# Kernel tuning notes

Measured on AMD Instinct MI355X. Metric: run time of the kernel, lower is better.

Reference implementation:

```python
import jax, jax.numpy as jnp
import numpy as np

NUM_GROUPS = 32
EPS = 1e-5


def group_norm(x, gamma, beta):
    # x: (b, c, h, w)
    b, c, h, w = x.shape
    xg = x.reshape(b, NUM_GROUPS, c // NUM_GROUPS, h, w)
    mean = xg.mean(axis=(2, 3, 4), keepdims=True)
    var = xg.var(axis=(2, 3, 4), keepdims=True)
    xn = ((xg - mean) * jax.lax.rsqrt(var + EPS)).reshape(b, c, h, w)
    return xn * gamma[None, :, None, None] + beta[None, :, None, None]


def conv1x1(x, w, b):
    # 1x1 conv == channel matmul: x (b,c,h,w), w (out,in), b (out,)
    return jnp.einsum('bchw,oc->bohw', x, w) + b[None, :, None, None]


def setup_inputs() -> dict:
    key = jax.random.key(0)
    ks = jax.random.split(key, 10)
    C = 512
    x = jax.random.normal(ks[0], (16, C, 32, 32), dtype=jnp.float32)
    s = 1.0 / np.sqrt(C)
    return {
        'x': x,
        'norm_w': jnp.ones((C,), jnp.float32),
        'norm_b': jnp.zeros((C,), jnp.float32),
        'q_w': jax.random.normal(ks[1], (C, C), jnp.float32) * s,
        'q_b': jax.random.normal(ks[2], (C,), jnp.float32) * 0.01,
        'k_w': jax.random.normal(ks[3], (C, C), jnp.float32) * s,
        'k_b': jax.random.normal(ks[4], (C,), jnp.float32) * 0.01,
        'v_w': jax.random.normal(ks[5], (C, C), jnp.float32) * s,
        'v_b': jax.random.normal(ks[6], (C,), jnp.float32) * 0.01,
        'proj_w': jax.random.normal(ks[7], (C, C), jnp.float32) * s,
        'proj_b': jax.random.normal(ks[8], (C,), jnp.float32) * 0.01,
    }


def reference(x, norm_w, norm_b, q_w, q_b, k_w, k_b, v_w, v_b, proj_w, proj_b):
    b, c, h, w = x.shape
    hn = group_norm(x, norm_w, norm_b)
    q = conv1x1(hn, q_w, q_b).reshape(b, c, h * w)  # (b, c, n)
    k = conv1x1(hn, k_w, k_b).reshape(b, c, h * w)
    v = conv1x1(hn, v_w, v_b).reshape(b, c, h * w)
    scale = jnp.float32(c) ** -0.5
    # scores[b, i, j] = sum_c q[b,c,i] * k[b,c,j]
    scores = jnp.einsum('bci,bcj->bij', q, k) * scale  # (b, n, n)
    attn = jax.nn.softmax(scores, axis=-1)
    # h_[b, c, i] = sum_j v[b,c,j] * attn[b,i,j]
    out = jnp.einsum('bcj,bij->bci', v, attn).reshape(b, c, h, w)
    return x + conv1x1(out, proj_w, proj_b)
```

## Files before the change

kernel.cpp:

```cpp
#include <hip/hip_runtime.h>

#define B_ 16
#define C_ 512
#define N_ 1024

typedef __attribute__((ext_vector_type(8))) short bf16x8_t;
typedef __attribute__((ext_vector_type(4))) float f32x4_t;

__device__ __forceinline__ unsigned short f2bf(float f) {
  unsigned int u = __float_as_uint(f);
  u += 0x7fffu + ((u >> 16) & 1u);
  return (unsigned short)(u >> 16);
}

__device__ __forceinline__ f32x4_t mfma16(bf16x8_t a, bf16x8_t b, f32x4_t c) {
  return __builtin_amdgcn_mfma_f32_16x16x32_bf16(a, b, c, 0, 0, 0);
}

__device__ __forceinline__ void gload_lds16(const void* g, void* l) {
  __builtin_amdgcn_global_load_lds(
      (const __attribute__((address_space(1))) unsigned int*)g,
      (__attribute__((address_space(3))) unsigned int*)l, 16, 0, 0);
}

__global__ __launch_bounds__(256) void castw_k(
    const float* __restrict__ qw, const float* __restrict__ kw,
    const float* __restrict__ vw, const float* __restrict__ pw,
    unsigned short* __restrict__ Wqkv, unsigned short* __restrict__ Wp) {
  int i = blockIdx.x * 256 + threadIdx.x;
  Wqkv[i] = f2bf(qw[i]);
  Wqkv[262144 + i] = f2bf(kw[i]);
  Wqkv[524288 + i] = f2bf(vw[i]);
  Wp[i] = f2bf(pw[i]);
}

__global__ __launch_bounds__(512, 1) void gn_fused_k(
    const float* __restrict__ x, const float* __restrict__ gw,
    const float* __restrict__ gb, unsigned short* __restrict__ hn) {
  int blk = blockIdx.x;
  int b = blk >> 4, gp = blk & 15;
  int t = threadIdx.x, lane = t & 63, wave = t >> 6;
  __shared__ float xs[32768];
  __shared__ float red[2][2][8];
  const float* xg = x + ((long)b * C_ + gp * 32) * N_;
  float s0 = 0.f, s20 = 0.f, s1 = 0.f, s21 = 0.f;
#pragma unroll
  for (int i = 0; i < 16; ++i) {
    int f4 = t + 512 * i;
    float4 v = ((const float4*)xg)[f4];
    float sum = v.x + v.y + v.z + v.w;
    float sq = v.x * v.x + v.y * v.y + v.z * v.z + v.w * v.w;
    if (i < 8) { s0 += sum; s20 += sq; } else { s1 += sum; s21 += sq; }
    int fi = f4 << 2;
    int c = fi >> 10, n = fi & 1023;
    int nx = n ^ (((c >> 3) & 3) << 4);
    *(float4*)&xs[(c << 10) + nx] = v;
  }
#pragma unroll
  for (int m = 1; m < 64; m <<= 1) {
    s0 += __shfl_xor(s0, m); s20 += __shfl_xor(s20, m);
    s1 += __shfl_xor(s1, m); s21 += __shfl_xor(s21, m);
  }
  if (lane == 0) {
    red[0][0][wave] = s0; red[1][0][wave] = s20;
    red[0][1][wave] = s1; red[1][1][wave] = s21;
  }
  __syncthreads();
  float m0 = 0.f, v0 = 0.f, m1 = 0.f, v1 = 0.f;
#pragma unroll
  for (int w = 0; w < 8; ++w) {
    m0 += red[0][0][w]; v0 += red[1][0][w];
    m1 += red[0][1][w]; v1 += red[1][1][w];
  }
  m0 *= (1.f / 16384.f); m1 *= (1.f / 16384.f);
  float rv0 = rsqrtf(v0 * (1.f / 16384.f) - m0 * m0 + 1e-5f);
  float rv1 = rsqrtf(v1 * (1.f / 16384.f) - m1 * m1 + 1e-5f);
  int q = t & 3;
  float mean = (q >> 1) ? m1 : m0, rv = (q >> 1) ? rv1 : rv0;
  float ga[8], be[8];
#pragma unroll
  for (int jj = 0; jj < 8; ++jj) {
    int gc = gp * 32 + q * 8 + jj;
    ga[jj] = gw[gc] * rv;
    be[jj] = gb[gc] - mean * ga[jj];
  }
  unsigned short* ob = hn + (long)b * N_ * C_ + gp * 32 + q * 8;
  int n0 = t >> 2;
  for (int it = 0; it < 8; ++it) {
    int n = n0 + (it << 7);
    int nsw = n ^ (q << 4);
    unsigned short us[8];
#pragma unroll
    for (int jj = 0; jj < 8; ++jj) {
      int c = q * 8 + jj;
      us[jj] = f2bf(xs[(c << 10) + nsw] * ga[jj] + be[jj]);
    }
    *(uint4*)(ob + (long)n * C_) = *(uint4*)us;
  }
}

__global__ __launch_bounds__(256) void gemm_qkv(
    const unsigned short* __restrict__ W, const unsigned short* __restrict__ HN,
    const float* __restrict__ qb, const float* __restrict__ kb,
    const float* __restrict__ vb, unsigned short* __restrict__ Q2,
    unsigned short* __restrict__ K2, unsigned short* __restrict__ V2,
    float scale) {
  int flat = blockIdx.x + 12 * (blockIdx.y + 8 * blockIdx.z);
  int nf = (flat & 7) * 192 + (flat >> 3);
  int bxi = nf % 12, rem = nf / 12;
  int byi = rem & 7, bz = rem >> 3;
  const unsigned short* Ab = W + (long)bxi * 128 * 512;
  const unsigned short* Bb = HN + (long)bz * N_ * C_ + (long)byi * 128 * 512;
  __shared__ char lds[32768];
  char* As = lds;
  char* Bs = lds + 16384;
  int tid = threadIdx.x;
  int lane = tid & 63, wave = tid >> 6;
  int wr = wave >> 1, wc = wave & 1;
  int lrow = lane & 15, kgrp = lane >> 4;
  f32x4_t acc[4][4];
#pragma unroll
  for (int i = 0; i < 4; ++i)
#pragma unroll
    for (int j = 0; j < 4; ++j) acc[i][j] = (f32x4_t){0.f, 0.f, 0.f, 0.f};

  int perm = (((lane & 7) ^ (lane >> 3)) << 3);
  const unsigned short* Asrc = Ab + (long)(wave * 32 + (lane >> 3)) * 512 + perm;
  const unsigned short* Bsrc = Bb + (long)(wave * 32 + (lane >> 3)) * 512 + perm;
  char* Adst = As + wave * 32 * 128;
  char* Bdst = Bs + wave * 32 * 128;

  for (int kt = 0; kt < 8; ++kt) {
    __syncthreads();
#pragma unroll
    for (int i = 0; i < 4; ++i) {
      gload_lds16(Asrc + (long)i * 8 * 512 + kt * 64, Adst + i * 1024);
      gload_lds16(Bsrc + (long)i * 8 * 512 + kt * 64, Bdst + i * 1024);
    }
    __syncthreads();
#pragma unroll
    for (int ks = 0; ks < 2; ++ks) {
      bf16x8_t af[4], bfv[4];
#pragma unroll
      for (int mi = 0; mi < 4; ++mi) {
        int r = wr * 64 + mi * 16 + lrow;
        int o = r * 128 + ks * 64 + kgrp * 16;
        o ^= (r & 7) << 4;
        af[mi] = *(bf16x8_t*)(As + o);
      }
#pragma unroll
      for (int ni = 0; ni < 4; ++ni) {
        int r = wc * 64 + ni * 16 + lrow;
        int o = r * 128 + ks * 64 + kgrp * 16;
        o ^= (r & 7) << 4;
        bfv[ni] = *(bf16x8_t*)(Bs + o);
      }
#pragma unroll
      for (int mi = 0; mi < 4; ++mi)
#pragma unroll
        for (int ni = 0; ni < 4; ++ni)
          acc[mi][ni] = mfma16(af[mi], bfv[ni], acc[mi][ni]);
    }
  }

  int slab = bxi >> 2;
  const float* bias = slab == 0 ? qb : (slab == 1 ? kb : vb);
  float scl = slab == 0 ? scale : 1.f;
  int rowloc = (bxi & 3) * 128 + wr * 64;
  int colbase = byi * 128 + wc * 64;
  unsigned short* ob =
      (slab == 0 ? Q2 : (slab == 1 ? K2 : V2)) + ((long)bz << 19);
#pragma unroll
  for (int mi = 0; mi < 4; ++mi) {
#pragma unroll
    for (int ni = 0; ni < 4; ++ni) {
      int row0 = rowloc + mi * 16 + kgrp * 4;
      int col = colbase + ni * 16 + lrow;
      unsigned short us[4];
#pragma unroll
      for (int rg = 0; rg < 4; ++rg)
        us[rg] = f2bf((acc[mi][ni][rg] + bias[row0 + rg]) * scl);
      if (slab < 2) {
        long off = ((long)(col >> 4) << 13) + ((long)(row0 >> 3) << 7) +
                   ((col & 15) << 3) + (row0 & 7);
        *(ushort4*)(ob + off) = make_ushort4(us[0], us[1], us[2], us[3]);
      } else {
        long base16 = ((long)(row0 >> 4) << 14) + ((long)(col >> 3) << 7) +
                      (col & 7) + (row0 & 15) * 8;
#pragma unroll
        for (int rg = 0; rg < 4; ++rg) ob[base16 + rg * 8] = us[rg];
      }
    }
  }
}

__global__ __launch_bounds__(512, 1) void attn_pv_k(
    const unsigned short* __restrict__ q2, const unsigned short* __restrict__ k2,
    const unsigned short* __restrict__ v2, unsigned short* __restrict__ ao) {
  int f = blockIdx.x;
  int b = f & 15, ib = f >> 4;
  int tid = threadIdx.x, lane = tid & 63, wave = tid >> 6;
  int lrow = lane & 15, kgrp = lane >> 4;
  __shared__ unsigned short P2[65536];
  __shared__ float red[2][8][64];
  {
    const unsigned short* qsrc =
        q2 + ((long)b << 19) + ((long)(ib * 4) << 13) + wave * 4096 + lane * 8;
    char* qdst = (char*)P2 + wave * 8192;
#pragma unroll
    for (int i = 0; i < 8; ++i) gload_lds16(qsrc + i * 512, qdst + i * 1024);
  }
  asm volatile("s_waitcnt vmcnt(0)" ::: "memory");
  __syncthreads();
  f32x4_t acc[4][8];
#pragma unroll
  for (int h = 0; h < 4; ++h)
#pragma unroll
    for (int t = 0; t < 8; ++t) acc[h][t] = (f32x4_t){0.f, 0.f, 0.f, 0.f};
  const unsigned short* kb =
      k2 + ((long)b << 19) + ((long)(wave * 8) << 13) + lane * 8;
  for (int ks = 0; ks < 16; ++ks) {
    bf16x8_t kf[8];
#pragma unroll
    for (int t = 0; t < 8; ++t)
      kf[t] = *(const bf16x8_t*)(kb + t * 8192 + ks * 512);
    bf16x8_t qa[4];
#pragma unroll
    for (int h = 0; h < 4; ++h)
      qa[h] = *(const bf16x8_t*)&P2[h * 8192 + ks * 512 + lane * 8];
    __builtin_amdgcn_s_setprio(1);
#pragma unroll
    for (int h = 0; h < 4; ++h)
#pragma unroll
      for (int t = 0; t < 8; ++t) acc[h][t] = mfma16(qa[h], kf[t], acc[h][t]);
    __builtin_amdgcn_s_setprio(0);
  }
  float mx[4][4];
#pragma unroll
  for (int h = 0; h < 4; ++h)
#pragma unroll
    for (int rg = 0; rg < 4; ++rg) mx[h][rg] = -1e30f;
#pragma unroll
  for (int h = 0; h < 4; ++h)
#pragma unroll
    for (int t = 0; t < 8; ++t)
#pragma unroll
      for (int rg = 0; rg < 4; ++rg) mx[h][rg] = fmaxf(mx[h][rg], acc[h][t][rg]);
#pragma unroll
  for (int m = 1; m < 16; m <<= 1)
#pragma unroll
    for (int h = 0; h < 4; ++h)
#pragma unroll
      for (int rg = 0; rg < 4; ++rg)
        mx[h][rg] = fmaxf(mx[h][rg], __shfl_xor(mx[h][rg], m));
  if (lrow == 0) {
#pragma unroll
    for (int h = 0; h < 4; ++h)
#pragma unroll
      for (int rg = 0; rg < 4; ++rg)
        red[0][wave][h * 16 + kgrp * 4 + rg] = mx[h][rg];
  }
  __syncthreads();
  float gm[4][4], sm[4][4];
#pragma unroll
  for (int h = 0; h < 4; ++h)
#pragma unroll
    for (int rg = 0; rg < 4; ++rg) {
      int r = h * 16 + kgrp * 4 + rg;
      float g0 = fmaxf(fmaxf(red[0][0][r], red[0][1][r]),
                       fmaxf(red[0][2][r], red[0][3][r]));
      float g1 = fmaxf(fmaxf(red[0][4][r], red[0][5][r]),
                       fmaxf(red[0][6][r], red[0][7][r]));
      gm[h][rg] = fmaxf(g0, g1);
      sm[h][rg] = 0.f;
    }
#pragma unroll
  for (int h = 0; h < 4; ++h)
#pragma unroll
    for (int t = 0; t < 8; ++t) {
      int j = wave * 128 + t * 16 + lrow;
      int jb = j >> 3;
      int ob = h * 16384 + jb * 128 + (j & 7);
      int cx = (jb & 7) << 3;
#pragma unroll
      for (int rg = 0; rg < 4; ++rg) {
        float p = __expf(acc[h][t][rg] - gm[h][rg]);
        sm[h][rg] += p;
        P2[ob + (((kgrp * 4 + rg) << 3) ^ cx)] = f2bf(p);
      }
    }
#pragma unroll
  for (int m = 1; m < 16; m <<= 1)
#pragma unroll
    for (int h = 0; h < 4; ++h)
#pragma unroll
      for (int rg = 0; rg < 4; ++rg) sm[h][rg] += __shfl_xor(sm[h][rg], m);
  if (lrow == 0) {
#pragma unroll
    for (int h = 0; h < 4; ++h)
#pragma unroll
      for (int rg = 0; rg < 4; ++rg)
        red[1][wave][h * 16 + kgrp * 4 + rg] = sm[h][rg];
  }
  __syncthreads();
  float inv[4][4];
#pragma unroll
  for (int h = 0; h < 4; ++h)
#pragma unroll
    for (int rg = 0; rg < 4; ++rg) {
      int r = h * 16 + kgrp * 4 + rg;
      float s0 = red[1][0][r] + red[1][1][r] + red[1][2][r] + red[1][3][r];
      float s1 = red[1][4][r] + red[1][5][r] + red[1][6][r] + red[1][7][r];
      inv[h][rg] = 1.f / (s0 + s1);
    }
  f32x4_t o[4][4];
#pragma unroll
  for (int h = 0; h < 4; ++h)
#pragma unroll
    for (int cf = 0; cf < 4; ++cf) o[h][cf] = (f32x4_t){0.f, 0.f, 0.f, 0.f};
  const unsigned short* vbp =
      v2 + ((long)b << 19) + ((long)(wave * 4) << 14) + lane * 8;
  for (int js = 0; js < 32; ++js) {
    bf16x8_t vf[4];
#pragma unroll
    for (int cf = 0; cf < 4; ++cf)
      vf[cf] = *(const bf16x8_t*)(vbp + cf * 16384 + js * 512);
    int jb = js * 4 + kgrp;
    int pox = ((lrow ^ (jb & 7)) << 3) + jb * 128;
    bf16x8_t pa[4];
#pragma unroll
    for (int h = 0; h < 4; ++h)
      pa[h] = *(const bf16x8_t*)&P2[h * 16384 + pox];
    __builtin_amdgcn_s_setprio(1);
#pragma unroll
    for (int h = 0; h < 4; ++h)
#pragma unroll
      for (int cf = 0; cf < 4; ++cf)
        o[h][cf] = mfma16(pa[h], vf[cf], o[h][cf]);
    __builtin_amdgcn_s_setprio(0);
  }
  unsigned short* aob = ao + ((long)(b * N_ + ib * 64)) * C_;
#pragma unroll
  for (int h = 0; h < 4; ++h)
#pragma unroll
    for (int cf = 0; cf < 4; ++cf) {
      int c = wave * 64 + cf * 16 + lrow;
#pragma unroll
      for (int rg = 0; rg < 4; ++rg) {
        int i = h * 16 + kgrp * 4 + rg;
        aob[(long)i * C_ + c] = f2bf(o[h][cf][rg] * inv[h][rg]);
      }
    }
}

__global__ __launch_bounds__(256) void gemm_proj(
    const unsigned short* __restrict__ A, const unsigned short* __restrict__ Bm,
    const float* __restrict__ bias, const float* __restrict__ resid,
    float* __restrict__ outp) {
  int flat = blockIdx.x + 4 * (blockIdx.y + 8 * blockIdx.z);
  int nf = (flat & 7) * 64 + (flat >> 3);
  int bxi = nf & 3, byi = (nf >> 2) & 7, bz = nf >> 5;
  const unsigned short* Ab = A + (long)bxi * 128 * 512;
  const unsigned short* Bb = Bm + (long)bz * N_ * C_ + (long)byi * 128 * 512;
  __shared__ char lds[32768];
  char* As = lds;
  char* Bs = lds + 16384;
  int tid = threadIdx.x;
  int lane = tid & 63, wave = tid >> 6;
  int wr = wave >> 1, wc = wave & 1;
  int lrow = lane & 15, kgrp = lane >> 4;
  f32x4_t acc[4][4];
#pragma unroll
  for (int i = 0; i < 4; ++i)
#pragma unroll
    for (int j = 0; j < 4; ++j) acc[i][j] = (f32x4_t){0.f, 0.f, 0.f, 0.f};

  int perm = (((lane & 7) ^ (lane >> 3)) << 3);
  const unsigned short* Asrc = Ab + (long)(wave * 32 + (lane >> 3)) * 512 + perm;
  const unsigned short* Bsrc = Bb + (long)(wave * 32 + (lane >> 3)) * 512 + perm;
  char* Adst = As + wave * 32 * 128;
  char* Bdst = Bs + wave * 32 * 128;

  for (int kt = 0; kt < 8; ++kt) {
    __syncthreads();
#pragma unroll
    for (int i = 0; i < 4; ++i) {
      gload_lds16(Asrc + (long)i * 8 * 512 + kt * 64, Adst + i * 1024);
      gload_lds16(Bsrc + (long)i * 8 * 512 + kt * 64, Bdst + i * 1024);
    }
    __syncthreads();
#pragma unroll
    for (int ks = 0; ks < 2; ++ks) {
      bf16x8_t af[4], bfv[4];
#pragma unroll
      for (int mi = 0; mi < 4; ++mi) {
        int r = wr * 64 + mi * 16 + lrow;
        int o = r * 128 + ks * 64 + kgrp * 16;
        o ^= (r & 7) << 4;
        af[mi] = *(bf16x8_t*)(As + o);
      }
#pragma unroll
      for (int ni = 0; ni < 4; ++ni) {
        int r = wc * 64 + ni * 16 + lrow;
        int o = r * 128 + ks * 64 + kgrp * 16;
        o ^= (r & 7) << 4;
        bfv[ni] = *(bf16x8_t*)(Bs + o);
      }
#pragma unroll
      for (int mi = 0; mi < 4; ++mi)
#pragma unroll
        for (int ni = 0; ni < 4; ++ni)
          acc[mi][ni] = mfma16(af[mi], bfv[ni], acc[mi][ni]);
    }
  }

  int rowbase = bxi * 128 + wr * 64;
  int colbase = byi * 128 + wc * 64;
  float* ob = outp + (long)bz * C_ * N_;
  const float* rb = resid + (long)bz * C_ * N_;
#pragma unroll
  for (int mi = 0; mi < 4; ++mi) {
#pragma unroll
    for (int ni = 0; ni < 4; ++ni) {
      int row0 = rowbase + mi * 16 + kgrp * 4;
      int col = colbase + ni * 16 + lrow;
#pragma unroll
      for (int rg = 0; rg < 4; ++rg) {
        int r = row0 + rg;
        ob[(long)r * N_ + col] =
            acc[mi][ni][rg] + bias[r] + rb[(long)r * N_ + col];
      }
    }
  }
}

extern "C" void kernel_launch(void* const* d_in, const int* in_sizes, int n_in,
                              void* d_out, int out_size, void* d_ws,
                              size_t ws_size, hipStream_t stream) {
  (void)in_sizes; (void)n_in; (void)out_size; (void)ws_size;
  const float* x = (const float*)d_in[0];
  const float* nw = (const float*)d_in[1];
  const float* nb = (const float*)d_in[2];
  const float* qw = (const float*)d_in[3];
  const float* qbias = (const float*)d_in[4];
  const float* kw = (const float*)d_in[5];
  const float* kbias = (const float*)d_in[6];
  const float* vw = (const float*)d_in[7];
  const float* vbias = (const float*)d_in[8];
  const float* pw = (const float*)d_in[9];
  const float* pbias = (const float*)d_in[10];
  float* out = (float*)d_out;

  char* ws = (char*)d_ws;
  unsigned short* WQKV = (unsigned short*)(ws + 0);
  unsigned short* Wp = (unsigned short*)(ws + 1572864);
  unsigned short* HN = (unsigned short*)(ws + 2097152);
  unsigned short* Q2 = (unsigned short*)(ws + 18874368);
  unsigned short* K2 = (unsigned short*)(ws + 35651584);
  unsigned short* V2 = (unsigned short*)(ws + 52428800);
  unsigned short* AO = (unsigned short*)(ws + 69206016);

  castw_k<<<1024, 256, 0, stream>>>(qw, kw, vw, pw, WQKV, Wp);
  gn_fused_k<<<256, 512, 0, stream>>>(x, nw, nb, HN);

  const float scale = 0.04419417382415922f;
  gemm_qkv<<<dim3(12, 8, B_), 256, 0, stream>>>(WQKV, HN, qbias, kbias, vbias,
                                                Q2, K2, V2, scale);
  attn_pv_k<<<256, 512, 0, stream>>>(Q2, K2, V2, AO);
  gemm_proj<<<dim3(4, 8, B_), 256, 0, stream>>>(Wp, AO, pbias, x, out);
}
```

Baseline: 112.9 us.

## Prefetch V fragments, use exp2 with log2e-folded scale, centralize softmax reductions

The PV loop now double-buffers V fragments in registers, loading the next step's data while the current MFMAs run, and is fully unrolled to hide global load latency. The softmax switches from __expf to exp2f, with log2(e) folded into the Q scale constant. The cross-wave max and sum reductions are done once by 64 threads into shared memory instead of redundantly by every thread, which costs two extra barriers. Register pressure rises from the prefetch buffers and the full unroll.

```diff
diff --git a/kernel.cpp b/kernel.cpp
--- a/kernel.cpp
+++ b/kernel.cpp
@@ -203,6 +203,7 @@
   int lrow = lane & 15, kgrp = lane >> 4;
   __shared__ unsigned short P2[65536];
   __shared__ float red[2][8][64];
+  __shared__ float gmr[64], invr[64];
   {
     const unsigned short* qsrc =
         q2 + ((long)b << 19) + ((long)(ib * 4) << 13) + wave * 4096 + lane * 8;
@@ -261,17 +262,19 @@
         red[0][wave][h * 16 + kgrp * 4 + rg] = mx[h][rg];
   }
   __syncthreads();
+  if (tid < 64) {
+    float g = red[0][0][tid];
+#pragma unroll
+    for (int w = 1; w < 8; ++w) g = fmaxf(g, red[0][w][tid]);
+    gmr[tid] = g;
+  }
+  __syncthreads();
   float gm[4][4], sm[4][4];
 #pragma unroll
   for (int h = 0; h < 4; ++h)
 #pragma unroll
     for (int rg = 0; rg < 4; ++rg) {
-      int r = h * 16 + kgrp * 4 + rg;
-      float g0 = fmaxf(fmaxf(red[0][0][r], red[0][1][r]),
-                       fmaxf(red[0][2][r], red[0][3][r]));
-      float g1 = fmaxf(fmaxf(red[0][4][r], red[0][5][r]),
-                       fmaxf(red[0][6][r], red[0][7][r]));
-      gm[h][rg] = fmaxf(g0, g1);
+      gm[h][rg] = gmr[h * 16 + kgrp * 4 + rg];
       sm[h][rg] = 0.f;
     }
 #pragma unroll
@@ -284,7 +287,7 @@
       int cx = (jb & 7) << 3;
 #pragma unroll
       for (int rg = 0; rg < 4; ++rg) {
-        float p = __expf(acc[h][t][rg] - gm[h][rg]);
+        float p = exp2f(acc[h][t][rg] - gm[h][rg]);
         sm[h][rg] += p;
         P2[ob + (((kgrp * 4 + rg) << 3) ^ cx)] = f2bf(p);
       }
@@ -303,28 +306,37 @@
         red[1][wave][h * 16 + kgrp * 4 + rg] = sm[h][rg];
   }
   __syncthreads();
+  if (tid < 64) {
+    float s = red[1][0][tid];
+#pragma unroll
+    for (int w = 1; w < 8; ++w) s += red[1][w][tid];
+    invr[tid] = 1.f / s;
+  }
+  __syncthreads();
   float inv[4][4];
 #pragma unroll
   for (int h = 0; h < 4; ++h)
 #pragma unroll
-    for (int rg = 0; rg < 4; ++rg) {
-      int r = h * 16 + kgrp * 4 + rg;
-      float s0 = red[1][0][r] + red[1][1][r] + red[1][2][r] + red[1][3][r];
-      float s1 = red[1][4][r] + red[1][5][r] + red[1][6][r] + red[1][7][r];
-      inv[h][rg] = 1.f / (s0 + s1);
-    }
+    for (int rg = 0; rg < 4; ++rg)
+      inv[h][rg] = invr[h * 16 + kgrp * 4 + rg];
   f32x4_t o[4][4];
 #pragma unroll
   for (int h = 0; h < 4; ++h)
 #pragma unroll
     for (int cf = 0; cf < 4; ++cf) o[h][cf] = (f32x4_t){0.f, 0.f, 0.f, 0.f};
-  const unsigned short* vbp =
-      v2 + ((long)b << 19) + ((long)(wave * 4) << 14) + lane * 8;
+  const char* vb2 =
+      (const char*)(v2 + ((long)b << 19) + ((long)(wave * 4) << 14)) + lane * 16;
+  bf16x8_t vc[4];
+#pragma unroll
+  for (int cf = 0; cf < 4; ++cf) vc[cf] = *(const bf16x8_t*)(vb2 + cf * 32768);
+#pragma unroll
   for (int js = 0; js < 32; ++js) {
-    bf16x8_t vf[4];
-#pragma unroll
-    for (int cf = 0; cf < 4; ++cf)
-      vf[cf] = *(const bf16x8_t*)(vbp + cf * 16384 + js * 512);
+    bf16x8_t vn[4];
+    if (js < 31) {
+#pragma unroll
+      for (int cf = 0; cf < 4; ++cf)
+        vn[cf] = *(const bf16x8_t*)(vb2 + cf * 32768 + (js + 1) * 1024);
+    }
     int jb = js * 4 + kgrp;
     int pox = ((lrow ^ (jb & 7)) << 3) + jb * 128;
     bf16x8_t pa[4];
@@ -336,8 +348,12 @@
     for (int h = 0; h < 4; ++h)
 #pragma unroll
       for (int cf = 0; cf < 4; ++cf)
-        o[h][cf] = mfma16(pa[h], vf[cf], o[h][cf]);
+        o[h][cf] = mfma16(pa[h], vc[cf], o[h][cf]);
     __builtin_amdgcn_s_setprio(0);
+    if (js < 31) {
+#pragma unroll
+      for (int cf = 0; cf < 4; ++cf) vc[cf] = vn[cf];
+    }
   }
   unsigned short* aob = ao + ((long)(b * N_ + ib * 64)) * C_;
 #pragma unroll
@@ -463,7 +479,7 @@
   castw_k<<<1024, 256, 0, stream>>>(qw, kw, vw, pw, WQKV, Wp);
   gn_fused_k<<<256, 512, 0, stream>>>(x, nw, nb, HN);
 
-  const float scale = 0.04419417382415922f;
+  const float scale = 0.06375871512f;
   gemm_qkv<<<dim3(12, 8, B_), 256, 0, stream>>>(WQKV, HN, qbias, kbias, vbias,
                                                 Q2, K2, V2, scale);
   attn_pv_k<<<256, 512, 0, stream>>>(Q2, K2, V2, AO);
```

Result: no change. 110.9 us (-1.8%).
